# Optimization experiments

Hardware: AMD Instinct MI355X
Metric: run time of the kernel (lower is better)

The kernel has to match this reference:

```python
import jax, jax.numpy as jnp
import numpy as np

S = 128            # image_size
NF = 64            # nf (channels)
B, N = 16, 1
DIM = S * S // 16  # 1024
HEADS = max(1, S // 16)  # 8
DH = DIM // HEADS  # 128


def setup_inputs() -> dict:
    key = jax.random.key(0)
    ks = jax.random.split(key, 10)
    sc = lambda fan_in: 1.0 / np.sqrt(fan_in)
    return {
        "x": jax.random.normal(ks[0], (B, N, NF, S, S), dtype=jnp.float32),
        "We": jax.random.uniform(ks[1], (DIM, S * S), jnp.float32, -sc(S * S), sc(S * S)),
        "be": jax.random.uniform(ks[2], (DIM,), jnp.float32, -sc(S * S), sc(S * S)),
        "pos": jax.random.normal(ks[3], (1, NF, DIM), dtype=jnp.float32),
        "Wq": jax.random.uniform(ks[4], (DIM, DIM), jnp.float32, -sc(DIM), sc(DIM)),
        "Wk": jax.random.uniform(ks[5], (NF, NF), jnp.float32, -sc(NF), sc(NF)),
        "Wv": jax.random.uniform(ks[6], (DIM, DIM), jnp.float32, -sc(DIM), sc(DIM)),
        "Wo": jax.random.uniform(ks[7], (S * S, DIM), jnp.float32, -sc(DIM), sc(DIM)),
        "bo": jax.random.uniform(ks[8], (S * S,), jnp.float32, -sc(DIM), sc(DIM)),
    }


def reference(x, We, be, pos, Wq, Wk, Wv, Wo, bo):
    b, n, C, H, W = x.shape
    bn = b * n
    xf = x.reshape(bn, C, H * W)                       # [BN, C, S^2]
    xe = jnp.einsum('bcp,dp->bcd', xf, We) + be + pos  # [BN, C, DIM]
    # q projection -> heads -> avgpool over head dim (AvgPool1d(dh) == mean)
    q = jnp.einsum('bcd,ed->bce', xe, Wq).reshape(bn, C, HEADS, DH)
    q = q.transpose(0, 2, 1, 3)                        # [BN, H, C, dh]
    q = q.mean(axis=-1)                                # [BN, H, C]
    k = jax.nn.sigmoid(jnp.einsum('bhc,fc->bhf', q, Wk))  # [BN, H, C]
    v = jnp.einsum('bcd,ed->bce', xe, Wv).reshape(bn, C, HEADS, DH)
    v = v.transpose(0, 2, 1, 3)                        # [BN, H, C, dh]
    # diag_embed(k) @ v == per-channel elementwise scale
    out = k[..., None] * v                             # [BN, H, C, dh]
    out = out.transpose(0, 2, 1, 3).reshape(bn, C, DIM)
    out = jnp.einsum('bcd,pd->bcp', out, Wo) + bo      # [BN, C, S^2]
    return out.reshape(b, n, C, H, W)
```

## Files before the change

### kernel.cpp

```cpp
#include <hip/hip_runtime.h>
#include <cstdint>
#include <cmath>


typedef __attribute__((ext_vector_type(8))) short short8;
typedef __attribute__((ext_vector_type(4))) float f32x4;

#define DIMD 1024
#define NCH  64
#define NHEAD 8
#define DHEAD 128

typedef __attribute__((address_space(1))) unsigned int gu32;
typedef __attribute__((address_space(3))) unsigned int lu32;

__device__ __forceinline__ void gload_lds16(const void* g, void* l) {
  __builtin_amdgcn_global_load_lds((gu32*)g, (lu32*)l, 16, 0, 0);
}

__device__ __forceinline__ unsigned short f2bf(float f) {
  union { float f; unsigned u; } a; a.f = f;
  unsigned u = a.u;
  unsigned r = (u + 0x7fffu + ((u >> 16) & 1u)) >> 16;
  return (unsigned short)r;
}
__device__ __forceinline__ float bf2f(unsigned short h) {
  union { unsigned u; float f; } a; a.u = ((unsigned)h) << 16; return a.f;
}

__device__ __forceinline__ uint4 pack8(float4 f0, float4 f1) {
  uint4 u;
  u.x = (unsigned)f2bf(f0.x) | ((unsigned)f2bf(f0.y) << 16);
  u.y = (unsigned)f2bf(f0.z) | ((unsigned)f2bf(f0.w) << 16);
  u.z = (unsigned)f2bf(f1.x) | ((unsigned)f2bf(f1.y) << 16);
  u.w = (unsigned)f2bf(f1.z) | ((unsigned)f2bf(f1.w) << 16);
  return u;
}

__device__ __forceinline__ void cvt8_body(const float* __restrict__ in,
                                          unsigned short* __restrict__ out, int i) {
  const float4* p = (const float4*)in + (size_t)i * 2;
  ((uint4*)out)[i] = pack8(p[0], p[1]);
}

__global__ __launch_bounds__(256) void cvt_bf16_kernel(
    const float* __restrict__ in, unsigned short* __restrict__ out, int n8) {
  int i = blockIdx.x * 256 + threadIdx.x;
  if (i >= n8) return;
  cvt8_body(in, out, i);
}

__global__ __launch_bounds__(256) void prep_fused(
    const float* __restrict__ x,  unsigned short* __restrict__ x_bf,
    const float* __restrict__ We, unsigned short* __restrict__ We_bf,
    const float* __restrict__ Wo, unsigned short* __restrict__ Wo_bf,
    const float* __restrict__ Wv, unsigned short* __restrict__ Wv_bf,
    const float* __restrict__ Wq, float* __restrict__ wqm) {
  int b = blockIdx.x;
  if (b < 8192) {
    cvt8_body(x, x_bf, b * 256 + threadIdx.x);
  } else if (b < 16384) {
    cvt8_body(We, We_bf, (b - 8192) * 256 + threadIdx.x);
  } else if (b < 24576) {
    cvt8_body(Wo, Wo_bf, (b - 16384) * 256 + threadIdx.x);
  } else if (b < 25088) {
    cvt8_body(Wv, Wv_bf, (b - 24576) * 256 + threadIdx.x);
  } else {
    int bb = b - 25088;
    int h = bb >> 3, dbase = (bb & 7) * 128;
    int d = threadIdx.x & 127, eh = threadIdx.x >> 7;
    const float* p = Wq + ((size_t)(h * DHEAD + eh * 64)) * DIMD + dbase + d;
    float s = 0.f;
    #pragma unroll 8
    for (int e = 0; e < 64; ++e) s += p[(size_t)e * DIMD];
    __shared__ float red[2][128];
    red[eh][d] = s;
    __syncthreads();
    if (eh == 0)
      wqm[h * DIMD + dbase + d] = (red[0][d] + red[1][d]) * (1.0f / DHEAD);
  }
}

__global__ __launch_bounds__(256) void wqm2_kernel(
    const float* __restrict__ Wq, float* __restrict__ wqm) {
  int h = blockIdx.x >> 3, dbase = (blockIdx.x & 7) * 128;
  int d = threadIdx.x & 127, eh = threadIdx.x >> 7;
  const float* p = Wq + ((size_t)(h * DHEAD + eh * 64)) * DIMD + dbase + d;
  float s = 0.f;
  #pragma unroll 8
  for (int e = 0; e < 64; ++e) s += p[(size_t)e * DIMD];
  __shared__ float red[2][128];
  red[eh][d] = s;
  __syncthreads();
  if (eh == 0)
    wqm[h * DIMD + dbase + d] = (red[0][d] + red[1][d]) * (1.0f / DHEAD);
}

__global__ __launch_bounds__(256) void qk2_kernel(
    const unsigned short* __restrict__ xe, const float* __restrict__ wqm,
    const float* __restrict__ Wk, float* __restrict__ kout) {
  int b = blockIdx.x, h = blockIdx.y;
  int c = threadIdx.x & 63, dq = threadIdx.x >> 6;
  __shared__ float red[64][4];
  __shared__ float qs[64];
  const uint4* xr = (const uint4*)(xe + ((size_t)(b * NCH + c)) * DIMD + dq * 256);
  const float* wr = wqm + h * DIMD + dq * 256;
  float s = 0.f;
  #pragma unroll 4
  for (int i = 0; i < 32; ++i) {
    uint4 v = xr[i];
    s += bf2f((unsigned short)(v.x & 0xffff)) * wr[i * 8 + 0];
    s += bf2f((unsigned short)(v.x >> 16))    * wr[i * 8 + 1];
    s += bf2f((unsigned short)(v.y & 0xffff)) * wr[i * 8 + 2];
    s += bf2f((unsigned short)(v.y >> 16))    * wr[i * 8 + 3];
    s += bf2f((unsigned short)(v.z & 0xffff)) * wr[i * 8 + 4];
    s += bf2f((unsigned short)(v.z >> 16))    * wr[i * 8 + 5];
    s += bf2f((unsigned short)(v.w & 0xffff)) * wr[i * 8 + 6];
    s += bf2f((unsigned short)(v.w >> 16))    * wr[i * 8 + 7];
  }
  red[c][dq] = s;
  __syncthreads();
  if (dq == 0) qs[c] = red[c][0] + red[c][1] + red[c][2] + red[c][3];
  __syncthreads();
  int f = c;
  float s2 = 0.f;
  #pragma unroll
  for (int i = 0; i < 16; ++i) {
    int cc = dq * 16 + i;
    s2 += qs[cc] * Wk[f * NCH + cc];
  }
  red[f][dq] = s2;
  __syncthreads();
  if (dq == 0) {
    float q = red[f][0] + red[f][1] + red[f][2] + red[f][3];
    kout[(b * NHEAD + h) * NCH + f] = 1.f / (1.f + expf(-q));
  }
}


#define BARR asm volatile("s_barrier" ::: "memory")
#define VMW(n) asm volatile("s_waitcnt vmcnt(" #n ")" ::: "memory")
#define LGKM0 asm volatile("s_waitcnt lgkmcnt(0)" ::: "memory")

#define SA(bb, kk, u) gload_lds16(gA + (size_t)(u) * 64 * K + (kk), \
                                  lA0 + (bb) * 16384 + (u) * 4096)
#define SB(bb, kk, u) gload_lds16(gB + (size_t)(u) * 64 * K + (kk), \
                                  lB0 + (bb) * 16384 + (u) * 4096)

template<int MODE, int LAYOUT>
__global__ __launch_bounds__(512, 2) void gemm8(
    const unsigned short* __restrict__ A, const unsigned short* __restrict__ Bg,
    float* __restrict__ C, const float* __restrict__ bias,
    int M, int N, int K, int Ksub)
{
  __shared__ __align__(16) unsigned short As[2][256][64];
  __shared__ __align__(16) unsigned short Bs[2][256][64];

  const int bid = blockIdx.x;
  int m0, n0, kz;
  if (LAYOUT == 1) {
    kz = (bid & 7) | (((bid >> 3) & 1) << 3);
    int r = bid >> 4; n0 = (r & 3) * 256; m0 = (r >> 2) * 256;
  } else {
    int nlo = bid & 7; int r = bid >> 3;
    m0 = (r & 3) * 256; n0 = (nlo + 8 * (r >> 2)) * 256; kz = 0;
  }
  const int kbeg = kz * Ksub;
  const int NT = Ksub >> 6;

  const int tid  = threadIdx.x;
  const int lane = tid & 63, wave = tid >> 6;
  const int wm = wave >> 2, wn = wave & 3;
  const int q = lane >> 4, rl = lane & 15;
  const int swz = rl & 7;

  const int srow = wave * 8 + (lane >> 3);
  const int kswz = ((lane & 7) ^ (lane >> 3)) << 3;
  const unsigned short* gA = A  + (size_t)(m0 + srow) * K + kbeg + kswz;
  const unsigned short* gB = Bg + (size_t)(n0 + srow) * K + kbeg + kswz;
  unsigned short* lA0 = &As[0][0][0] + wave * 512;
  unsigned short* lB0 = &Bs[0][0][0] + wave * 512;

  f32x4 acc[8][4] = {};

  SA(0, 0, 0); SA(0, 0, 1); SA(0, 0, 2); SA(0, 0, 3);
  SB(0, 0, 0); SB(0, 0, 1); SB(0, 0, 2); SB(0, 0, 3);
  VMW(0);
  BARR;

  const int g0 = (q ^ swz) << 3;
  const int g1 = ((4 | q) ^ swz) << 3;

  for (int t = 0; t < NT; ++t) {
    const int buf = t & 1, nb = buf ^ 1;
    if (t + 1 < NT) {
      const size_t kn = (size_t)(t + 1) * 64;
      SA(nb, kn, 0); SA(nb, kn, 1); SA(nb, kn, 2); SA(nb, kn, 3);
      SB(nb, kn, 0); SB(nb, kn, 1); SB(nb, kn, 2); SB(nb, kn, 3);
    }
    const unsigned short* ap = &As[buf][wm * 128 + rl][0];
    const unsigned short* bp = &Bs[buf][wn * 64 + rl][0];

    short8 a0[8], b0[4];
    #pragma unroll
    for (int mi = 0; mi < 8; ++mi)
      a0[mi] = *(const short8*)(ap + mi * 1024 + g0);
    #pragma unroll
    for (int nj = 0; nj < 4; ++nj)
      b0[nj] = *(const short8*)(bp + nj * 1024 + g0);
    LGKM0;
    __builtin_amdgcn_sched_barrier(0);
    __builtin_amdgcn_s_setprio(1);
    #pragma unroll
    for (int mi = 0; mi < 8; ++mi)
      #pragma unroll
      for (int nj = 0; nj < 4; ++nj)
        acc[mi][nj] = __builtin_amdgcn_mfma_f32_16x16x32_bf16(a0[mi], b0[nj], acc[mi][nj], 0, 0, 0);
    __builtin_amdgcn_s_setprio(0);

    short8 a1[8], b1[4];
    #pragma unroll
    for (int mi = 0; mi < 8; ++mi)
      a1[mi] = *(const short8*)(ap + mi * 1024 + g1);
    #pragma unroll
    for (int nj = 0; nj < 4; ++nj)
      b1[nj] = *(const short8*)(bp + nj * 1024 + g1);
    LGKM0;
    __builtin_amdgcn_sched_barrier(0);
    __builtin_amdgcn_s_setprio(1);
    #pragma unroll
    for (int mi = 0; mi < 8; ++mi)
      #pragma unroll
      for (int nj = 0; nj < 4; ++nj)
        acc[mi][nj] = __builtin_amdgcn_mfma_f32_16x16x32_bf16(a1[mi], b1[nj], acc[mi][nj], 0, 0, 0);
    __builtin_amdgcn_s_setprio(0);

    VMW(0);
    __builtin_amdgcn_sched_barrier(0);
    BARR;
  }

  const size_t zoff = (MODE == 3) ? (size_t)kz * (size_t)M * (size_t)N : 0;
  #pragma unroll
  for (int mi = 0; mi < 8; ++mi) {
    #pragma unroll
    for (int nj = 0; nj < 4; ++nj) {
      #pragma unroll
      for (int r = 0; r < 4; ++r) {
        int row = m0 + wm * 128 + mi * 16 + q * 4 + r;
        int col = n0 + wn * 64 + nj * 16 + rl;
        if (MODE == 3) {
          C[zoff + (size_t)row * N + col] = acc[mi][nj][r];
        } else {
          C[(size_t)row * N + col] = acc[mi][nj][r] + bias[col];
        }
      }
    }
  }
}

template<int MODE, int LAYOUT>
__global__ __launch_bounds__(256) void gemm_db(
    const unsigned short* __restrict__ A, const unsigned short* __restrict__ B,
    float* __restrict__ C, const float* __restrict__ bias,
    int M, int N, int K, int Ksub)
{
  __shared__ __align__(16) unsigned short As[2][128][32];
  __shared__ __align__(16) unsigned short Bs[2][128][32];

  const int bid = blockIdx.x;
  int m0, n0, kz;
  if (LAYOUT == 0) {
    kz = bid & 7; int r = bid >> 3; n0 = (r & 7) * 128; m0 = (r >> 3) * 128;
  } else if (LAYOUT == 1) {
    kz = (bid & 7) | (((bid >> 3) & 1) << 3);
    int r = bid >> 4; n0 = (r & 7) * 128; m0 = (r >> 3) * 128;
  } else {
    int nlo = bid & 7, nhi = bid >> 6;
    m0 = ((bid >> 3) & 7) * 128; n0 = (nlo + 8 * nhi) * 128; kz = 0;
  }

  const int tid  = threadIdx.x;
  const int lane = tid & 63, wave = tid >> 6;
  const int kbeg = kz * Ksub;
  const int lrow = lane >> 2;
  const int lcol = (lane & 3) * 8;
  const int q = lane >> 4, rl = lane & 15;
  const int wr = (wave >> 1) * 64, wc = (wave & 1) * 64;

  const unsigned short* ga = A + (size_t)(m0 + wave * 32 + lrow) * K + kbeg + lcol;
  const unsigned short* gb = B + (size_t)(n0 + wave * 32 + lrow) * K + kbeg + lcol;

  f32x4 acc[4][4] = {};

  gload_lds16(ga,                  &As[0][wave * 32][0]);
  gload_lds16(ga + (size_t)16 * K, &As[0][wave * 32 + 16][0]);
  gload_lds16(gb,                  &Bs[0][wave * 32][0]);
  gload_lds16(gb + (size_t)16 * K, &Bs[0][wave * 32 + 16][0]);
  ga += 32; gb += 32;

  int p = 0;
  for (int k0 = 0; k0 < Ksub; k0 += 32) {
    __syncthreads();
    if (k0 + 32 < Ksub) {
      gload_lds16(ga,                  &As[p ^ 1][wave * 32][0]);
      gload_lds16(ga + (size_t)16 * K, &As[p ^ 1][wave * 32 + 16][0]);
      gload_lds16(gb,                  &Bs[p ^ 1][wave * 32][0]);
      gload_lds16(gb + (size_t)16 * K, &Bs[p ^ 1][wave * 32 + 16][0]);
      ga += 32; gb += 32;
    }

    short8 af[4], bf[4];
    #pragma unroll
    for (int i = 0; i < 4; ++i)
      af[i] = *(const short8*)&As[p][wr + i * 16 + rl][q * 8];
    #pragma unroll
    for (int j = 0; j < 4; ++j)
      bf[j] = *(const short8*)&Bs[p][wc + j * 16 + rl][q * 8];
    #pragma unroll
    for (int i = 0; i < 4; ++i)
      #pragma unroll
      for (int j = 0; j < 4; ++j)
        acc[i][j] = __builtin_amdgcn_mfma_f32_16x16x32_bf16(af[i], bf[j], acc[i][j], 0, 0, 0);

    p ^= 1;
  }

  const size_t zoff = (MODE == 3) ? (size_t)kz * (size_t)M * (size_t)N : 0;
  #pragma unroll
  for (int i = 0; i < 4; ++i) {
    #pragma unroll
    for (int j = 0; j < 4; ++j) {
      #pragma unroll
      for (int r = 0; r < 4; ++r) {
        int row = m0 + wr + i * 16 + q * 4 + r;
        int col = n0 + wc + j * 16 + rl;
        if (MODE == 3) {
          C[zoff + (size_t)row * N + col] = acc[i][j][r];
        } else {
          C[(size_t)row * N + col] = acc[i][j][r] + bias[col];
        }
      }
    }
  }
}

template<int NS>
__global__ __launch_bounds__(256) void reduce1_kernel(
    const float* __restrict__ part, const float* __restrict__ be,
    const float* __restrict__ pos, unsigned short* __restrict__ xe) {
  int i = blockIdx.x * 256 + threadIdx.x;
  size_t base = (size_t)i * 4;
  int row = i >> 8, col = (i & 255) * 4;
  float4 s = {0.f, 0.f, 0.f, 0.f};
  #pragma unroll
  for (int sk = 0; sk < NS; ++sk) {
    float4 p = *(const float4*)(part + (size_t)sk * (DIMD * DIMD) + base);
    s.x += p.x; s.y += p.y; s.z += p.z; s.w += p.w;
  }
  float4 bv = *(const float4*)(be + col);
  float4 pv = *(const float4*)(pos + (size_t)(row & 63) * DIMD + col);
  uint2 u;
  u.x = (unsigned)f2bf(s.x + bv.x + pv.x) | ((unsigned)f2bf(s.y + bv.y + pv.y) << 16);
  u.y = (unsigned)f2bf(s.z + bv.z + pv.z) | ((unsigned)f2bf(s.w + bv.w + pv.w) << 16);
  *(uint2*)(xe + base) = u;
}

template<int NS>
__global__ __launch_bounds__(256) void reduce2_kernel(
    const float* __restrict__ part, const float* __restrict__ kv,
    unsigned short* __restrict__ t) {
  int i = blockIdx.x * 256 + threadIdx.x;
  size_t base = (size_t)i * 4;
  int row = i >> 8, col = (i & 255) * 4;
  float4 s = {0.f, 0.f, 0.f, 0.f};
  #pragma unroll
  for (int sk = 0; sk < NS; ++sk) {
    float4 p = *(const float4*)(part + (size_t)sk * (DIMD * DIMD) + base);
    s.x += p.x; s.y += p.y; s.z += p.z; s.w += p.w;
  }
  float sc = kv[((row >> 6) * NHEAD + (col >> 7)) * NCH + (row & 63)];
  uint2 u;
  u.x = (unsigned)f2bf(s.x * sc) | ((unsigned)f2bf(s.y * sc) << 16);
  u.y = (unsigned)f2bf(s.z * sc) | ((unsigned)f2bf(s.w * sc) << 16);
  *(uint2*)(t + base) = u;
}

template<int MODE, bool ABF16, int BM, int BN>
__global__ __launch_bounds__(256) void gemm_bt(
    const void* __restrict__ Ap, const float* __restrict__ B,
    void* __restrict__ C, const float* __restrict__ bias,
    const float* __restrict__ posp, const float* __restrict__ ksc,
    int M, int N, int K)
{
  constexpr int BK = 32;
  constexpr int LDR = BK + 8;
  __shared__ __align__(16) unsigned short As[BM][LDR];
  __shared__ __align__(16) unsigned short Bs[BN][LDR];

  const int tid = threadIdx.x;
  const int m0 = blockIdx.y * BM;
  const int n0 = blockIdx.x * BN;
  constexpr int EA = BM * BK / 256;
  constexpr int EB = BN * BK / 256;
  constexpr int MI = BM / 32;
  constexpr int NI = BN / 32;
  const int lane = tid & 63, wave = tid >> 6;
  const int wr = (wave >> 1) * (BM / 2);
  const int wc = (wave & 1) * (BN / 2);
  const int q = lane >> 4, rl = lane & 15;

  f32x4 acc[MI][NI] = {};

  for (int k0 = 0; k0 < K; k0 += BK) {
    {
      constexpr int CPR = BK / EA;
      int row = tid / CPR;
      int cs  = (tid % CPR) * EA;
      if (ABF16) {
        const unsigned short* a = (const unsigned short*)Ap + (size_t)(m0 + row) * K + k0 + cs;
        #pragma unroll
        for (int v = 0; v < EA / 8; ++v)
          *(uint4*)&As[row][cs + v * 8] = *(const uint4*)(a + v * 8);
      } else {
        const float* a = (const float*)Ap + (size_t)(m0 + row) * K + k0 + cs;
        #pragma unroll
        for (int v = 0; v < EA / 8; ++v) {
          float4 f0 = *(const float4*)(a + v * 8);
          float4 f1 = *(const float4*)(a + v * 8 + 4);
          *(uint4*)&As[row][cs + v * 8] = pack8(f0, f1);
        }
      }
    }
    {
      constexpr int CPR = BK / EB;
      int row = tid / CPR;
      int cs  = (tid % CPR) * EB;
      const float* b = B + (size_t)(n0 + row) * K + k0 + cs;
      #pragma unroll
      for (int v = 0; v < EB / 8; ++v) {
        float4 f0 = *(const float4*)(b + v * 8);
        float4 f1 = *(const float4*)(b + v * 8 + 4);
        *(uint4*)&Bs[row][cs + v * 8] = pack8(f0, f1);
      }
    }
    __syncthreads();

    short8 af[MI], bf[NI];
    #pragma unroll
    for (int i = 0; i < MI; ++i)
      af[i] = *(const short8*)&As[wr + i * 16 + rl][q * 8];
    #pragma unroll
    for (int j = 0; j < NI; ++j)
      bf[j] = *(const short8*)&Bs[wc + j * 16 + rl][q * 8];
    #pragma unroll
    for (int i = 0; i < MI; ++i)
      #pragma unroll
      for (int j = 0; j < NI; ++j)
        acc[i][j] = __builtin_amdgcn_mfma_f32_16x16x32_bf16(af[i], bf[j], acc[i][j], 0, 0, 0);

    __syncthreads();
  }

  #pragma unroll
  for (int i = 0; i < MI; ++i) {
    #pragma unroll
    for (int j = 0; j < NI; ++j) {
      #pragma unroll
      for (int r = 0; r < 4; ++r) {
        int row = m0 + wr + i * 16 + q * 4 + r;
        int col = n0 + wc + j * 16 + rl;
        float v = acc[i][j][r];
        if (MODE == 0) {
          v += bias[col] + posp[(size_t)(row & 63) * DIMD + col];
          ((unsigned short*)C)[(size_t)row * N + col] = f2bf(v);
        } else if (MODE == 1) {
          v *= ksc[((row >> 6) * NHEAD + (col >> 7)) * NCH + (row & 63)];
          ((unsigned short*)C)[(size_t)row * N + col] = f2bf(v);
        } else {
          ((float*)C)[(size_t)row * N + col] = v + bias[col];
        }
      }
    }
  }
}

__global__ void wqm_kernel(const float* __restrict__ Wq, float* __restrict__ wqm) {
  int h = blockIdx.x;
  for (int d = threadIdx.x; d < DIMD; d += 256) {
    float s = 0.f;
    const float* p = Wq + (size_t)h * DHEAD * DIMD + d;
    #pragma unroll 4
    for (int e = 0; e < DHEAD; ++e) s += p[(size_t)e * DIMD];
    wqm[h * DIMD + d] = s * (1.0f / DHEAD);
  }
}
__global__ void qk_kernel(const unsigned short* __restrict__ xe,
                          const float* __restrict__ wqm,
                          const float* __restrict__ Wk,
                          float* __restrict__ kout) {
  int b = blockIdx.x;
  __shared__ float qs[NHEAD][NCH];
  for (int t = threadIdx.x; t < NHEAD * NCH; t += 256) {
    int h = t >> 6, c = t & 63;
    const unsigned short* xr = xe + (size_t)(b * NCH + c) * DIMD;
    const float* wr = wqm + h * DIMD;
    float s = 0.f;
    #pragma unroll 8
    for (int d = 0; d < DIMD; ++d) s += bf2f(xr[d]) * wr[d];
    qs[h][c] = s;
  }
  __syncthreads();
  for (int t = threadIdx.x; t < NHEAD * NCH; t += 256) {
    int h = t >> 6, f = t & 63;
    float s = 0.f;
    #pragma unroll
    for (int c = 0; c < NCH; ++c) s += qs[h][c] * Wk[f * NCH + c];
    kout[b * (NHEAD * NCH) + h * NCH + f] = 1.f / (1.f + expf(-s));
  }
}

extern "C" void kernel_launch(void* const* d_in, const int* in_sizes, int n_in,
                              void* d_out, int out_size, void* d_ws, size_t ws_size,
                              hipStream_t stream) {
  const float* x   = (const float*)d_in[0];
  const float* We  = (const float*)d_in[1];
  const float* be  = (const float*)d_in[2];
  const float* pos = (const float*)d_in[3];
  const float* Wq  = (const float*)d_in[4];
  const float* Wk  = (const float*)d_in[5];
  const float* Wv  = (const float*)d_in[6];
  const float* Wo  = (const float*)d_in[7];
  const float* bo  = (const float*)d_in[8];
  float* out = (float*)d_out;

  const size_t MB = 1u << 20;
  const size_t WS16 = 102 * MB + 64 * 1024;
  const size_t WS8  = 70 * MB + 64 * 1024;

  if (ws_size >= WS16) {
    char* ws = (char*)d_ws;
    unsigned short* We_bf = (unsigned short*)(ws + 0);
    unsigned short* Wo_bf = (unsigned short*)(ws + 32 * MB);
    unsigned short* x_bf  = (unsigned short*)(ws + 64 * MB);
    unsigned short* Wv_bf = (unsigned short*)(ws + 96 * MB);
    unsigned short* xe    = (unsigned short*)(ws + 98 * MB);
    unsigned short* t     = (unsigned short*)(ws + 100 * MB);
    float* wqm = (float*)(ws + 102 * MB);
    float* kv  = (float*)(ws + 102 * MB + 32 * 1024);

    float* part1 = (float*)d_out;
    float* part2 = (float*)d_out;

    prep_fused<<<dim3(25152), 256, 0, stream>>>(
        x, x_bf, We, We_bf, Wo, Wo_bf, Wv, Wv_bf, Wq, wqm);

    gemm8<3, 1><<<dim3(256), 512, 0, stream>>>(
        x_bf, We_bf, part1, nullptr, 1024, 1024, 16384, 1024);
    reduce1_kernel<16><<<dim3(1024), 256, 0, stream>>>(part1, be, pos, xe);

    qk2_kernel<<<dim3(16, 8), 256, 0, stream>>>(xe, wqm, Wk, kv);

    gemm_db<3, 0><<<dim3(512), 256, 0, stream>>>(
        xe, Wv_bf, part2, nullptr, 1024, 1024, 1024, 128);
    reduce2_kernel<8><<<dim3(1024), 256, 0, stream>>>(part2, kv, t);

    gemm8<2, 2><<<dim3(256), 512, 0, stream>>>(
        t, Wo_bf, out, bo, 1024, 16384, 1024, 1024);
  } else if (ws_size >= WS8) {
    char* ws = (char*)d_ws;
    unsigned short* We_bf = (unsigned short*)(ws + 0);
    unsigned short* Wo_bf = (unsigned short*)(ws + 32 * MB);
    unsigned short* Wv_bf = (unsigned short*)(ws + 64 * MB);
    unsigned short* xe    = (unsigned short*)(ws + 66 * MB);
    unsigned short* t     = (unsigned short*)(ws + 68 * MB);
    float* wqm = (float*)(ws + 70 * MB);
    float* kv  = (float*)(ws + 70 * MB + 32 * 1024);

    char* ob = (char*)d_out;
    unsigned short* x_bf  = (unsigned short*)(ob + 0);
    float* part1 = (float*)(ob + 32 * MB);
    float* part2 = (float*)(ob + 0);

    cvt_bf16_kernel<<<dim3(8192), 256, 0, stream>>>(x,  x_bf,  16777216 / 8);
    cvt_bf16_kernel<<<dim3(8192), 256, 0, stream>>>(We, We_bf, 16777216 / 8);
    cvt_bf16_kernel<<<dim3(512),  256, 0, stream>>>(Wv, Wv_bf, 1048576 / 8);
    cvt_bf16_kernel<<<dim3(8192), 256, 0, stream>>>(Wo, Wo_bf, 16777216 / 8);
    wqm2_kernel<<<dim3(64), 256, 0, stream>>>(Wq, wqm);

    gemm_db<3, 0><<<dim3(512), 256, 0, stream>>>(
        x_bf, We_bf, part1, nullptr, 1024, 1024, 16384, 2048);
    reduce1_kernel<8><<<dim3(1024), 256, 0, stream>>>(part1, be, pos, xe);

    qk2_kernel<<<dim3(16, 8), 256, 0, stream>>>(xe, wqm, Wk, kv);

    gemm_db<3, 0><<<dim3(512), 256, 0, stream>>>(
        xe, Wv_bf, part2, nullptr, 1024, 1024, 1024, 128);
    reduce2_kernel<8><<<dim3(1024), 256, 0, stream>>>(part2, kv, t);

    gemm_db<2, 2><<<dim3(1024), 256, 0, stream>>>(
        t, Wo_bf, out, bo, 1024, 16384, 1024, 1024);
  } else {
    char* ws = (char*)d_ws;
    unsigned short* xe = (unsigned short*)ws;
    unsigned short* t  = (unsigned short*)(ws + (2u << 20));
    float* wqm = (float*)(ws + (4u << 20));
    float* kv  = (float*)(ws + (4u << 20) + (32u << 10));

    wqm_kernel<<<dim3(NHEAD), 256, 0, stream>>>(Wq, wqm);
    gemm_bt<0, false, 64, 64><<<dim3(16, 16), 256, 0, stream>>>(
        x, We, xe, be, pos, nullptr, 1024, 1024, 16384);
    qk_kernel<<<dim3(16), 256, 0, stream>>>(xe, wqm, Wk, kv);
    gemm_bt<1, true, 64, 64><<<dim3(16, 16), 256, 0, stream>>>(
        xe, Wv, t, nullptr, nullptr, kv, 1024, 1024, 1024);
    gemm_bt<2, true, 128, 128><<<dim3(128, 8), 256, 0, stream>>>(
        t, Wo, out, bo, nullptr, nullptr, 1024, 16384, 1024);
  }
}
```

Baseline: 354.8 us.

## Convert fp32 to bf16 with persistent waves streaming through LDS via async loads

The prep kernel used to launch about 25k small blocks, each converting 8 floats per thread. It now runs 512 persistent blocks whose waves each stream 32 KB slabs of x, We and Wo through double-buffered LDS, using global_load_lds with vmcnt waits to overlap loading with conversion. This is meant to cut block launch overhead and keep more loads in flight on a bandwidth-bound conversion, at the cost of fewer blocks, which may limit memory parallelism.

```diff
diff --git a/kernel.cpp b/kernel.cpp
--- a/kernel.cpp
+++ b/kernel.cpp
@@ -50,23 +50,66 @@
   cvt8_body(in, out, i);
 }
 
-__global__ __launch_bounds__(256) void prep_fused(
+#define VMW(n) asm volatile("s_waitcnt vmcnt(" #n ")" ::: "memory")
+
+__global__ __launch_bounds__(256) void prep5(
     const float* __restrict__ x,  unsigned short* __restrict__ x_bf,
     const float* __restrict__ We, unsigned short* __restrict__ We_bf,
     const float* __restrict__ Wo, unsigned short* __restrict__ Wo_bf,
     const float* __restrict__ Wv, unsigned short* __restrict__ Wv_bf,
     const float* __restrict__ Wq, float* __restrict__ wqm) {
   int b = blockIdx.x;
-  if (b < 8192) {
-    cvt8_body(x, x_bf, b * 256 + threadIdx.x);
-  } else if (b < 16384) {
-    cvt8_body(We, We_bf, (b - 8192) * 256 + threadIdx.x);
-  } else if (b < 24576) {
-    cvt8_body(Wo, Wo_bf, (b - 16384) * 256 + threadIdx.x);
-  } else if (b < 25088) {
-    cvt8_body(Wv, Wv_bf, (b - 24576) * 256 + threadIdx.x);
+  if (b < 512) {
+    __shared__ __align__(16) unsigned short slab_s[4][8192];
+    const int wave = threadIdx.x >> 6, lane = threadIdx.x & 63;
+    const int w = b * 4 + wave;
+    unsigned short* slab = &slab_s[wave][0];
+
+#define P5_SRC(r) ((r) < 4 ? x : (r) < 8 ? We : Wo)
+#define P5_DSTP(r) ((r) < 4 ? x_bf : (r) < 8 ? We_bf : Wo_bf)
+#define P5_ISSUE(r) do { \
+      const float* s_ = P5_SRC(r) + (size_t)w * 8192 + ((r) & 3) * 2048 + lane * 4; \
+      unsigned short* l_ = slab + ((r) & 1) * 4096; \
+      _Pragma("unroll") \
+      for (int j_ = 0; j_ < 8; ++j_) \
+        gload_lds16(s_ + j_ * 256, l_ + j_ * 512); \
+    } while (0)
+
+    P5_ISSUE(0);
+    #pragma unroll
+    for (int r = 0; r < 12; ++r) {
+      if (r + 1 < 12) {
+        switch (r + 1) {
+        case 1: P5_ISSUE(1); break;  case 2: P5_ISSUE(2); break;
+        case 3: P5_ISSUE(3); break;  case 4: P5_ISSUE(4); break;
+        case 5: P5_ISSUE(5); break;  case 6: P5_ISSUE(6); break;
+        case 7: P5_ISSUE(7); break;  case 8: P5_ISSUE(8); break;
+        case 9: P5_ISSUE(9); break;  case 10: P5_ISSUE(10); break;
+        case 11: P5_ISSUE(11); break;
+        }
+        VMW(8);
+      } else {
+        VMW(0);
+      }
+      unsigned short* dp = P5_DSTP(r) + (size_t)w * 8192 + (r & 3) * 2048;
+      const unsigned short* lb = slab + (r & 1) * 4096;
+      #pragma unroll
+      for (int j = 0; j < 8; ++j) {
+        float4 f = *(const float4*)(lb + j * 512 + lane * 8);
+        uint2 u;
+        u.x = (unsigned)f2bf(f.x) | ((unsigned)f2bf(f.y) << 16);
+        u.y = (unsigned)f2bf(f.z) | ((unsigned)f2bf(f.w) << 16);
+        *(uint2*)(dp + j * 256 + lane * 4) = u;
+      }
+    }
+#undef P5_ISSUE
+#undef P5_DSTP
+#undef P5_SRC
+  } else if (b < 1024) {
+    int gid = (b - 512) * 256 + threadIdx.x;
+    cvt8_body(Wv, Wv_bf, gid);
   } else {
-    int bb = b - 25088;
+    int bb = b - 1024;
     int h = bb >> 3, dbase = (bb & 7) * 128;
     int d = threadIdx.x & 127, eh = threadIdx.x >> 7;
     const float* p = Wq + ((size_t)(h * DHEAD + eh * 64)) * DIMD + dbase + d;
@@ -139,7 +182,6 @@
 
 
 #define BARR asm volatile("s_barrier" ::: "memory")
-#define VMW(n) asm volatile("s_waitcnt vmcnt(" #n ")" ::: "memory")
 #define LGKM0 asm volatile("s_waitcnt lgkmcnt(0)" ::: "memory")
 
 #define SA(bb, kk, u) gload_lds16(gA + (size_t)(u) * 64 * K + (kk), \
@@ -552,7 +594,7 @@
     float* part1 = (float*)d_out;
     float* part2 = (float*)d_out;
 
-    prep_fused<<<dim3(25152), 256, 0, stream>>>(
+    prep5<<<dim3(1088), 256, 0, stream>>>(
         x, x_bf, We, We_bf, Wo, Wo_bf, Wv, Wv_bf, Wq, wqm);
 
     gemm8<3, 1><<<dim3(256), 512, 0, stream>>>(
```

Result: slower. 362.1 us (+2.1%).

## Fuse fp32-to-bf16 conversion of x, We, Wo into GEMM tile loads

Applied to the files above, without the earlier changes.

Drops the separate pass that converted x, We and Wo to bf16 in workspace. The first and last GEMMs now read fp32 tiles straight into registers, pack them to bf16 and store them into LDS, staggering the A and B loads across the two MFMA half-steps. This removes a large write and re-read of bf16 copies. In exchange, the GEMMs read twice the bytes per operand, give up direct global-to-LDS loads, and raise register pressure under a 512-thread, 2-block launch bound.

```diff
diff --git a/kernel.cpp b/kernel.cpp
--- a/kernel.cpp
+++ b/kernel.cpp
@@ -50,23 +50,14 @@
   cvt8_body(in, out, i);
 }
 
-__global__ __launch_bounds__(256) void prep_fused(
-    const float* __restrict__ x,  unsigned short* __restrict__ x_bf,
-    const float* __restrict__ We, unsigned short* __restrict__ We_bf,
-    const float* __restrict__ Wo, unsigned short* __restrict__ Wo_bf,
+__global__ __launch_bounds__(256) void prep6(
     const float* __restrict__ Wv, unsigned short* __restrict__ Wv_bf,
     const float* __restrict__ Wq, float* __restrict__ wqm) {
   int b = blockIdx.x;
-  if (b < 8192) {
-    cvt8_body(x, x_bf, b * 256 + threadIdx.x);
-  } else if (b < 16384) {
-    cvt8_body(We, We_bf, (b - 8192) * 256 + threadIdx.x);
-  } else if (b < 24576) {
-    cvt8_body(Wo, Wo_bf, (b - 16384) * 256 + threadIdx.x);
-  } else if (b < 25088) {
-    cvt8_body(Wv, Wv_bf, (b - 24576) * 256 + threadIdx.x);
+  if (b < 512) {
+    cvt8_body(Wv, Wv_bf, b * 256 + threadIdx.x);
   } else {
-    int bb = b - 25088;
+    int bb = b - 512;
     int h = bb >> 3, dbase = (bb & 7) * 128;
     int d = threadIdx.x & 127, eh = threadIdx.x >> 7;
     const float* p = Wq + ((size_t)(h * DHEAD + eh * 64)) * DIMD + dbase + d;
@@ -142,14 +133,27 @@
 #define VMW(n) asm volatile("s_waitcnt vmcnt(" #n ")" ::: "memory")
 #define LGKM0 asm volatile("s_waitcnt lgkmcnt(0)" ::: "memory")
 
-#define SA(bb, kk, u) gload_lds16(gA + (size_t)(u) * 64 * K + (kk), \
-                                  lA0 + (bb) * 16384 + (u) * 4096)
-#define SB(bb, kk, u) gload_lds16(gB + (size_t)(u) * 64 * K + (kk), \
-                                  lB0 + (bb) * 16384 + (u) * 4096)
-
-template<int MODE, int LAYOUT>
-__global__ __launch_bounds__(512, 2) void gemm8(
-    const unsigned short* __restrict__ A, const unsigned short* __restrict__ Bg,
+#define SA16(bb, kk, u) gload_lds16(gA16 + (size_t)(u) * 64 * K + (kk), \
+                                    lA0 + (bb) * 16384 + (u) * 4096)
+#define SB16(bb, kk, u) gload_lds16(gB16 + (size_t)(u) * 64 * K + (kk), \
+                                    lB0 + (bb) * 16384 + (u) * 4096)
+#define LDF(dst, src, kk) do { _Pragma("unroll") \
+  for (int u_ = 0; u_ < 4; ++u_) { \
+    dst[u_ * 2]     = *(const float4*)(src + (size_t)u_ * 64 * K + (kk)); \
+    dst[u_ * 2 + 1] = *(const float4*)(src + (size_t)u_ * 64 * K + (kk) + 4); \
+  } } while (0)
+#define WRA(bb) do { _Pragma("unroll") \
+  for (int u_ = 0; u_ < 4; ++u_) \
+    *(uint4*)(&As[bb][0][0] + u_ * 4096 + wave * 512 + lane * 8) = \
+        pack8(fA[u_ * 2], fA[u_ * 2 + 1]); } while (0)
+#define WRB(bb) do { _Pragma("unroll") \
+  for (int u_ = 0; u_ < 4; ++u_) \
+    *(uint4*)(&Bs[bb][0][0] + u_ * 4096 + wave * 512 + lane * 8) = \
+        pack8(fB[u_ * 2], fB[u_ * 2 + 1]); } while (0)
+
+template<int MODE, int LAYOUT, bool AF32, bool BF32>
+__global__ __launch_bounds__(512, 2) void gemm8f(
+    const void* __restrict__ Ap, const void* __restrict__ Bp,
     float* __restrict__ C, const float* __restrict__ bias,
     int M, int N, int K, int Ksub)
 {
@@ -175,17 +179,30 @@
   const int swz = rl & 7;
 
   const int srow = wave * 8 + (lane >> 3);
-  const int kswz = ((lane & 7) ^ (lane >> 3)) << 3;
-  const unsigned short* gA = A  + (size_t)(m0 + srow) * K + kbeg + kswz;
-  const unsigned short* gB = Bg + (size_t)(n0 + srow) * K + kbeg + kswz;
+  const int gg   = (lane & 7) ^ (lane >> 3);
+  const int kswz = gg << 3;
+  const unsigned short* gA16 = AF32 ? nullptr
+      : (const unsigned short*)Ap + (size_t)(m0 + srow) * K + kbeg + kswz;
+  const unsigned short* gB16 = BF32 ? nullptr
+      : (const unsigned short*)Bp + (size_t)(n0 + srow) * K + kbeg + kswz;
+  const float* gA32 = AF32
+      ? (const float*)Ap + (size_t)(m0 + srow) * K + kbeg + kswz : nullptr;
+  const float* gB32 = BF32
+      ? (const float*)Bp + (size_t)(n0 + srow) * K + kbeg + kswz : nullptr;
   unsigned short* lA0 = &As[0][0][0] + wave * 512;
   unsigned short* lB0 = &Bs[0][0][0] + wave * 512;
 
   f32x4 acc[8][4] = {};
-
-  SA(0, 0, 0); SA(0, 0, 1); SA(0, 0, 2); SA(0, 0, 3);
-  SB(0, 0, 0); SB(0, 0, 1); SB(0, 0, 2); SB(0, 0, 3);
-  VMW(0);
+  float4 fA[8], fB[8];
+
+  if (AF32) { LDF(fA, gA32, 0); }
+  else { SA16(0, 0, 0); SA16(0, 0, 1); SA16(0, 0, 2); SA16(0, 0, 3); }
+  if (BF32) { LDF(fB, gB32, 0); }
+  else { SB16(0, 0, 0); SB16(0, 0, 1); SB16(0, 0, 2); SB16(0, 0, 3); }
+  if (AF32 && BF32)      { VMW(8); WRA(0); VMW(0); WRB(0); LGKM0; }
+  else if (AF32)         { VMW(0); WRA(0); LGKM0; }
+  else if (BF32)         { VMW(0); WRB(0); LGKM0; }
+  else                   { VMW(0); }
   BARR;
 
   const int g0 = (q ^ swz) << 3;
@@ -193,10 +210,12 @@
 
   for (int t = 0; t < NT; ++t) {
     const int buf = t & 1, nb = buf ^ 1;
-    if (t + 1 < NT) {
-      const size_t kn = (size_t)(t + 1) * 64;
-      SA(nb, kn, 0); SA(nb, kn, 1); SA(nb, kn, 2); SA(nb, kn, 3);
-      SB(nb, kn, 0); SB(nb, kn, 1); SB(nb, kn, 2); SB(nb, kn, 3);
+    const bool s = (t + 1) < NT;
+    const size_t kn = (size_t)(t + 1) * 64;
+
+    if (s) {
+      if (AF32) { LDF(fA, gA32, kn); }
+      else { SA16(nb, kn, 0); SA16(nb, kn, 1); SA16(nb, kn, 2); SA16(nb, kn, 3); }
     }
     const unsigned short* ap = &As[buf][wm * 128 + rl][0];
     const unsigned short* bp = &Bs[buf][wn * 64 + rl][0];
@@ -218,6 +237,11 @@
         acc[mi][nj] = __builtin_amdgcn_mfma_f32_16x16x32_bf16(a0[mi], b0[nj], acc[mi][nj], 0, 0, 0);
     __builtin_amdgcn_s_setprio(0);
 
+    if (s) {
+      if (BF32) { LDF(fB, gB32, kn); }
+      else { SB16(nb, kn, 0); SB16(nb, kn, 1); SB16(nb, kn, 2); SB16(nb, kn, 3); }
+    }
+
     short8 a1[8], b1[4];
     #pragma unroll
     for (int mi = 0; mi < 8; ++mi)
@@ -235,7 +259,15 @@
         acc[mi][nj] = __builtin_amdgcn_mfma_f32_16x16x32_bf16(a1[mi], b1[nj], acc[mi][nj], 0, 0, 0);
     __builtin_amdgcn_s_setprio(0);
 
-    VMW(0);
+    if (s) {
+      if (AF32 && BF32) { VMW(8); WRA(nb); VMW(0); WRB(nb); }
+      else if (AF32)    { VMW(0); WRA(nb); }
+      else if (BF32)    { VMW(0); WRB(nb); }
+      else              { VMW(0); }
+      LGKM0;
+    } else {
+      VMW(0);
+    }
     __builtin_amdgcn_sched_barrier(0);
     BARR;
   }
@@ -540,9 +572,6 @@
 
   if (ws_size >= WS16) {
     char* ws = (char*)d_ws;
-    unsigned short* We_bf = (unsigned short*)(ws + 0);
-    unsigned short* Wo_bf = (unsigned short*)(ws + 32 * MB);
-    unsigned short* x_bf  = (unsigned short*)(ws + 64 * MB);
     unsigned short* Wv_bf = (unsigned short*)(ws + 96 * MB);
     unsigned short* xe    = (unsigned short*)(ws + 98 * MB);
     unsigned short* t     = (unsigned short*)(ws + 100 * MB);
@@ -552,11 +581,10 @@
     float* part1 = (float*)d_out;
     float* part2 = (float*)d_out;
 
-    prep_fused<<<dim3(25152), 256, 0, stream>>>(
-        x, x_bf, We, We_bf, Wo, Wo_bf, Wv, Wv_bf, Wq, wqm);
-
-    gemm8<3, 1><<<dim3(256), 512, 0, stream>>>(
-        x_bf, We_bf, part1, nullptr, 1024, 1024, 16384, 1024);
+    prep6<<<dim3(576), 256, 0, stream>>>(Wv, Wv_bf, Wq, wqm);
+
+    gemm8f<3, 1, true, true><<<dim3(256), 512, 0, stream>>>(
+        x, We, part1, nullptr, 1024, 1024, 16384, 1024);
     reduce1_kernel<16><<<dim3(1024), 256, 0, stream>>>(part1, be, pos, xe);
 
     qk2_kernel<<<dim3(16, 8), 256, 0, stream>>>(xe, wqm, Wk, kv);
@@ -565,8 +593,8 @@
         xe, Wv_bf, part2, nullptr, 1024, 1024, 1024, 128);
     reduce2_kernel<8><<<dim3(1024), 256, 0, stream>>>(part2, kv, t);
 
-    gemm8<2, 2><<<dim3(256), 512, 0, stream>>>(
-        t, Wo_bf, out, bo, 1024, 16384, 1024, 1024);
+    gemm8f<2, 2, false, true><<<dim3(256), 512, 0, stream>>>(
+        t, Wo, out, bo, 1024, 16384, 1024, 1024);
   } else if (ws_size >= WS8) {
     char* ws = (char*)d_ws;
     unsigned short* We_bf = (unsigned short*)(ws + 0);
```

After: 528.9 us. +49.1%, slower.
